# Kernel tuning notes

Measured on AMD Instinct MI355X. Metric: run time of the kernel, lower is better.

## Reference

```python
import jax, jax.numpy as jnp
import numpy as np

H = 768   # encoder hidden size
NH = 4    # boundary attention heads
HD = H // NH
E = 9     # ent_type_size
R = 12    # rel_type_size
D = 64    # inner_dim
B = 4
S = 1024


def setup_inputs() -> dict:
    key = jax.random.key(0)
    ks = jax.random.split(key, 8)
    n = lambda k, shp: jax.random.normal(k, shp, jnp.float32) * 0.02
    return dict(
        hidden_states=jax.random.normal(ks[0], (B, S, H), jnp.float32),
        attention_mask=jnp.ones((B, S), jnp.float32),
        in_proj_w=n(ks[1], (3 * H, H)), in_proj_b=jnp.zeros((3 * H,), jnp.float32),
        out_proj_w=n(ks[2], (H, H)), out_proj_b=jnp.zeros((H,), jnp.float32),
        gate_w=n(ks[3], (H, H)), gate_b=jnp.zeros((H,), jnp.float32),
        ln_g=jnp.ones((H,), jnp.float32), ln_b=jnp.zeros((H,), jnp.float32),
        ent_w=n(ks[4], (E * 2 * D, H)), ent_b=jnp.zeros((E * 2 * D,), jnp.float32),
        prior_w=n(ks[5], (H, E)), prior_b=jnp.zeros((H,), jnp.float32),
        rel_w=n(ks[6], (R * 2 * D, 2 * H)), rel_b=jnp.zeros((R * 2 * D,), jnp.float32),
    )


def _sinusoidal_pos_emb(seq_len, dim, dtype):
    pos = jnp.arange(seq_len, dtype=dtype)[:, None]                 # [S,1]
    inv = jnp.power(jnp.asarray(10000.0, dtype), -2.0 * jnp.arange(dim // 2, dtype=dtype) / dim)
    ang = pos * inv                                                  # [S,D/2]
    emb = jnp.stack([jnp.sin(ang), jnp.cos(ang)], axis=-1).reshape(seq_len, dim)  # [sin0,cos0,sin1,cos1,...]
    return emb


def _gp_matrix(hs, W, b, mask):
    # hs: [B,S,Hin], W: [T*2D, Hin], mask: [B,S]
    bsz, seq_len, _ = hs.shape
    out = hs @ W.T + b                                               # [B,S,T*2D]
    T = out.shape[-1] // (2 * D)
    out = out.reshape(bsz, seq_len, T, 2 * D)
    qw, kw = out[..., :D], out[..., D:]                              # [B,S,T,D]
    # RoPE
    pe = _sinusoidal_pos_emb(seq_len, D, hs.dtype)                   # [S,D]
    cos = jnp.repeat(pe[:, 1::2], 2, axis=-1)[None, :, None, :]      # [1,S,1,D]
    sin = jnp.repeat(pe[:, ::2], 2, axis=-1)[None, :, None, :]

    def rot(x):
        x2 = jnp.stack([-x[..., 1::2], x[..., ::2]], axis=-1).reshape(x.shape)
        return x * cos + x2 * sin

    qw, kw = rot(qw), rot(kw)
    logits = jnp.einsum('bmtd,bntd->btmn', qw, kw)                   # [B,T,S,S]
    pad = mask[:, None, None, :]                                     # masks key dim
    logits = logits * pad - (1.0 - pad) * 1e12
    tril = jnp.tril(jnp.ones((seq_len, seq_len), logits.dtype), -1)
    logits = logits - tril * 1e12                                    # strictly lower triangle masked
    return logits / jnp.sqrt(jnp.asarray(D, logits.dtype))


def _boundary_attention(hs, mask, in_proj_w, in_proj_b, out_proj_w, out_proj_b,
                        gate_w, gate_b, ln_g, ln_b):
    bsz, seq_len, _ = hs.shape
    qkv = hs @ in_proj_w.T + in_proj_b                               # [B,S,3H]
    q, k, v = jnp.split(qkv, 3, axis=-1)
    q = q.reshape(bsz, seq_len, NH, HD)
    k = k.reshape(bsz, seq_len, NH, HD)
    v = v.reshape(bsz, seq_len, NH, HD)
    scores = jnp.einsum('bqhd,bkhd->bhqk', q, k) / jnp.sqrt(jnp.asarray(HD, hs.dtype))
    key_pad = (mask == 0)[:, None, None, :]                          # [B,1,1,S]
    scores = jnp.where(key_pad, jnp.asarray(-1e9, hs.dtype), scores)
    attn = jax.nn.softmax(scores, axis=-1)
    ctx = jnp.einsum('bhqk,bkhd->bqhd', attn, v).reshape(bsz, seq_len, H)
    attn_out = ctx @ out_proj_w.T + out_proj_b
    gate = jax.nn.sigmoid(attn_out @ gate_w.T + gate_b)
    x = hs + gate * attn_out
    mu = jnp.mean(x, axis=-1, keepdims=True)
    var = jnp.var(x, axis=-1, keepdims=True)
    return (x - mu) / jnp.sqrt(var + 1e-5) * ln_g + ln_b


def reference(hidden_states, attention_mask, in_proj_w, in_proj_b, out_proj_w, out_proj_b,
              gate_w, gate_b, ln_g, ln_b, ent_w, ent_b, prior_w, prior_b, rel_w, rel_b):
    enhanced = _boundary_attention(hidden_states, attention_mask, in_proj_w, in_proj_b,
                                   out_proj_w, out_proj_b, gate_w, gate_b, ln_g, ln_b)
    ent_logits = _gp_matrix(enhanced, ent_w, ent_b, attention_mask)  # [B,E,S,S]
    ent_prior = jnp.max(ent_logits, axis=-1)                          # [B,E,S]
    ent_prior = jnp.swapaxes(ent_prior, 1, 2)                         # [B,S,E]
    prior_feat = jax.nn.relu(ent_prior @ prior_w.T + prior_b)         # [B,S,H]
    rel_hidden = jnp.concatenate([enhanced, prior_feat], axis=-1)     # [B,S,2H]
    rel_logits = _gp_matrix(rel_hidden, rel_w, rel_b, attention_mask) # [B,R,S,S]
    return (ent_logits, rel_logits, enhanced)
```

## Files before the change

### kernel.cpp

```cpp
#include <hip/hip_runtime.h>
#include <math.h>

#define H_   768
#define NH_  4
#define HD_  192
#define E_   9
#define R_   12
#define D_   64
#define B_   4
#define S_   1024
#define H3_  (3 * H_)
#define MBS_ (B_ * S_)

typedef unsigned short u16;
typedef __attribute__((ext_vector_type(4))) int   i32x4;
typedef __attribute__((ext_vector_type(4))) float f32x4;

static const long OUT_REL_OFF = (long)B_ * E_ * S_ * S_;
static const long OUT_ENH_OFF = OUT_REL_OFF + (long)B_ * R_ * S_ * S_;

__device__ __forceinline__ u16 f2bf(float f) {
    unsigned u = __builtin_bit_cast(unsigned, f);
    return (u16)((u + 0x7fffu + ((u >> 16) & 1u)) >> 16);
}
__device__ __forceinline__ float bf2f(u16 h) {
    return __builtin_bit_cast(float, (unsigned)h << 16);
}
__device__ __forceinline__ void gload16(const u16* g, u16* l) {
    __builtin_amdgcn_global_load_lds(
        (__attribute__((address_space(1))) void*)g,
        (__attribute__((address_space(3))) void*)l, 16, 0, 0);
}
__device__ __forceinline__ void mfma_bf16(f32x4& acc, i32x4 a, i32x4 b) {
    asm volatile("v_mfma_f32_16x16x32_bf16 %0, %1, %2, %0"
                 : "+v"(acc) : "v"(a), "v"(b));
}

template<int BM, int BN, int EPI, int OBF, int PIPE>
__global__ __launch_bounds__(256) void gemm_mfma(
    const u16* __restrict__ A, const u16* __restrict__ Bw,
    const float* __restrict__ bias, void* __restrict__ Cv,
    int K, int lda, int ldb, int ldc, int nh,
    long sAb, long sAh, long sBb, long sBh, long sCb, long sCh,
    const float* __restrict__ mask, float scale, float* __restrict__ aux)
{
    constexpr int MI = BM / 32, NJ = BN / 32;
    constexpr int BUFE = (BM + BN) * 64;
    constexpr int LPS  = BM / 32 + BN / 32;
    const int z = blockIdx.z;
    const int zb = z / nh, zh = z - zb * nh;
    A  += zb * sAb + zh * sAh;
    Bw += zb * sBb + zh * sBh;

    const int gx = gridDim.x, gy = gridDim.y;
    int id = blockIdx.y * gx + blockIdx.x;
    const int nwg = gx * gy;
    if ((nwg & 7) == 0) id = (id & 7) * (nwg >> 3) + (id >> 3);
    const int bx = id % gx, by = id / gx;
    const int m0 = by * BM, n0 = bx * BN;

    __shared__ u16 lds[(PIPE ? 2 : 1) * BUFE];

    const int t = threadIdx.x;
    const int lane = t & 63, wid = t >> 6;
    const int wr = wid >> 1, wc = wid & 1;
    const int l16 = lane & 15, l4 = lane >> 4;

    auto stage = [&](int kt, u16* la) {
        u16* lb = la + BM * 64;
        const int k0 = kt << 6;
        #pragma unroll
        for (int i = 0; i < BM / 32; ++i) {
            const int e = i * 256 + t;
            const int row = e >> 3;
            const int c = ((e & 7) ^ (row & 7)) << 3;
            gload16(A + (long)(m0 + row) * lda + k0 + c, la + e * 8);
        }
        #pragma unroll
        for (int i = 0; i < BN / 32; ++i) {
            const int e = i * 256 + t;
            const int row = e >> 3;
            const int c = ((e & 7) ^ (row & 7)) << 3;
            gload16(Bw + (long)(n0 + row) * ldb + k0 + c, lb + e * 8);
        }
    };

    f32x4 acc[MI][NJ];
    #pragma unroll
    for (int mi = 0; mi < MI; ++mi)
        #pragma unroll
        for (int nj = 0; nj < NJ; ++nj)
            #pragma unroll
            for (int q = 0; q < 4; ++q) acc[mi][nj][q] = 0.0f;

    const int nt = K >> 6;

    if (PIPE == 0) {
        stage(0, lds);
        __syncthreads();
        const u16* la = lds;
        const u16* lb = lds + BM * 64;
        i32x4 af[MI][2], bfr[NJ][2];
        #pragma unroll
        for (int mi = 0; mi < MI; ++mi)
            #pragma unroll
            for (int kk = 0; kk < 2; ++kk) {
                const int row = wr * (BM / 2) + mi * 16 + l16;
                af[mi][kk] = *(const i32x4*)&la[row * 64 + ((((kk << 2) + l4) ^ (row & 7)) << 3)];
            }
        #pragma unroll
        for (int nj = 0; nj < NJ; ++nj)
            #pragma unroll
            for (int kk = 0; kk < 2; ++kk) {
                const int row = wc * (BN / 2) + nj * 16 + l16;
                bfr[nj][kk] = *(const i32x4*)&lb[row * 64 + ((((kk << 2) + l4) ^ (row & 7)) << 3)];
            }
        #pragma unroll
        for (int kk = 0; kk < 2; ++kk)
            #pragma unroll
            for (int mi = 0; mi < MI; ++mi)
                #pragma unroll
                for (int nj = 0; nj < NJ; ++nj)
                    mfma_bf16(acc[mi][nj], af[mi][kk], bfr[nj][kk]);
    } else {
        stage(0, lds);
        if (nt > 1) stage(1, lds + BUFE);
        for (int tt = 0; tt < nt; ++tt) {
            if (tt + 1 < nt) {
                if constexpr (LPS == 8) asm volatile("s_waitcnt vmcnt(8)" ::: "memory");
                else if constexpr (LPS == 7) asm volatile("s_waitcnt vmcnt(7)" ::: "memory");
                else if constexpr (LPS == 6) asm volatile("s_waitcnt vmcnt(6)" ::: "memory");
                else asm volatile("s_waitcnt vmcnt(5)" ::: "memory");
            } else {
                asm volatile("s_waitcnt vmcnt(0)" ::: "memory");
            }
            __builtin_amdgcn_s_barrier();
            u16* la = lds + (tt & 1) * BUFE;
            const u16* lb = la + BM * 64;
            i32x4 af[MI][2], bfr[NJ][2];
            #pragma unroll
            for (int mi = 0; mi < MI; ++mi)
                #pragma unroll
                for (int kk = 0; kk < 2; ++kk) {
                    const int row = wr * (BM / 2) + mi * 16 + l16;
                    af[mi][kk] = *(const i32x4*)&la[row * 64 + ((((kk << 2) + l4) ^ (row & 7)) << 3)];
                }
            #pragma unroll
            for (int nj = 0; nj < NJ; ++nj)
                #pragma unroll
                for (int kk = 0; kk < 2; ++kk) {
                    const int row = wc * (BN / 2) + nj * 16 + l16;
                    bfr[nj][kk] = *(const i32x4*)&lb[row * 64 + ((((kk << 2) + l4) ^ (row & 7)) << 3)];
                }
            asm volatile("s_waitcnt lgkmcnt(0)" ::: "memory");
            __builtin_amdgcn_sched_barrier(0);
            __builtin_amdgcn_s_barrier();
            if (tt + 2 < nt) stage(tt + 2, la);
            #pragma unroll
            for (int kk = 0; kk < 2; ++kk)
                #pragma unroll
                for (int mi = 0; mi < MI; ++mi)
                    #pragma unroll
                    for (int nj = 0; nj < NJ; ++nj)
                        mfma_bf16(acc[mi][nj], af[mi][kk], bfr[nj][kk]);
        }
        __syncthreads();
    }
    __builtin_amdgcn_sched_barrier(0);
    asm volatile("s_nop 7");
    asm volatile("s_nop 7");
    __builtin_amdgcn_sched_barrier(0);

    if (EPI == 1 || EPI == 3 || EPI == 5) mask += (long)zb * S_;
    const long cbase = zb * sCb + zh * sCh;

    float* sminv = (float*)lds;
    if (EPI == 6) {
        if (t < BM) {
            const float* pp = aux + ((long)z * S_ + m0 + t) * 16;
            float s = 0.0f;
            #pragma unroll
            for (int i = 0; i < 16; ++i) s += pp[i];
            sminv[t] = 1.0f / s;
        }
        __syncthreads();
    }

    float red[MI][4];
    if (EPI == 3 || EPI == 5) {
        #pragma unroll
        for (int mi = 0; mi < MI; ++mi)
            #pragma unroll
            for (int r = 0; r < 4; ++r) red[mi][r] = (EPI == 3) ? -INFINITY : 0.0f;
    }

    #pragma unroll
    for (int mi = 0; mi < MI; ++mi) {
        #pragma unroll
        for (int nj = 0; nj < NJ; ++nj) {
            const int gn = n0 + wc * (BN / 2) + nj * 16 + l16;
            const float bv = ((EPI == 0 || EPI == 4 || EPI == 7) && bias) ? bias[gn] : 0.0f;
            float invf = 0.0f;
            if (EPI == 4) invf = exp2f(-(float)((gn & 63) >> 1) * 0.41524101186092503f);
            #pragma unroll
            for (int r = 0; r < 4; ++r) {
                const int gm = m0 + wr * (BM / 2) + mi * 16 + l4 * 4 + r;
                float v = acc[mi][nj][r];
                const long cidx = cbase + (long)gm * ldc + gn;
                if (EPI == 0) {
                    v += bv;
                    if (OBF) ((u16*)Cv)[cidx] = f2bf(v);
                    else     ((float*)Cv)[cidx] = v;
                } else if (EPI == 7) {
                    v += bv;
                    const u16 bfv = f2bf(v);
                    ((u16*)Cv)[cidx] = bfv;
                    if (gn >= 2 * H_) {
                        const int hh = (gn - 2 * H_) / HD_;
                        const int dd = (gn - 2 * H_) - hh * HD_;
                        const int bb = gm >> 10, ss = gm & (S_ - 1);
                        ((u16*)aux)[((long)(bb * NH_ + hh) * HD_ + dd) * S_ + ss] = bfv;
                    }
                } else if (EPI == 1 || EPI == 3) {
                    const float pad = mask[gn];
                    v = v * pad - (1.0f - pad) * 1e12f;
                    if (gm > gn) v -= 1e12f;
                    v *= 0.125f;
                    ((float*)Cv)[cidx] = v;
                    if (EPI == 3) red[mi][r] = fmaxf(red[mi][r], v);
                } else if (EPI == 5) {
                    float tv = 0.0f;
                    if (mask[gn] != 0.0f) tv = __expf(v * scale);
                    ((u16*)Cv)[cidx] = f2bf(tv);
                    red[mi][r] += tv;
                } else if (EPI == 6) {
                    v *= sminv[gm - m0];
                    ((u16*)Cv)[cidx] = f2bf(v);
                } else {
                    v += bv;
                    const int sp = gm & (S_ - 1);
                    float sn, cs;
                    __sincosf((float)sp * invf, &sn, &cs);
                    const float pv = __shfl_xor(v, 1, 64);
                    v = (gn & 1) ? fmaf(v, cs, pv * sn) : fmaf(v, cs, -pv * sn);
                    ((u16*)Cv)[cidx] = f2bf(v);
                }
            }
        }
    }

    if (EPI == 3 || EPI == 5) {
        #pragma unroll
        for (int mi = 0; mi < MI; ++mi) {
            #pragma unroll
            for (int r = 0; r < 4; ++r) {
                float m = red[mi][r];
                if (EPI == 3) {
                    m = fmaxf(m, __shfl_xor(m, 1, 64));
                    m = fmaxf(m, __shfl_xor(m, 2, 64));
                    m = fmaxf(m, __shfl_xor(m, 4, 64));
                    m = fmaxf(m, __shfl_xor(m, 8, 64));
                } else {
                    m += __shfl_xor(m, 1, 64);
                    m += __shfl_xor(m, 2, 64);
                    m += __shfl_xor(m, 4, 64);
                    m += __shfl_xor(m, 8, 64);
                }
                if (l16 == 0) {
                    const int gm = m0 + wr * (BM / 2) + mi * 16 + l4 * 4 + r;
                    aux[((long)z * S_ + gm) * 16 + bx * 2 + wc] = m;
                }
            }
        }
    }
}

__global__ __launch_bounds__(256) void cast_all(
    const float* __restrict__ hs, const float* __restrict__ ipw,
    const float* __restrict__ opw, const float* __restrict__ gw,
    const float* __restrict__ entw, const float* __restrict__ relw,
    u16* hs_o, u16* ipw_o, u16* opw_o, u16* gw_o, u16* entw_o, u16* relw_o)
{
    const int blk = blockIdx.x;
    const float* in; u16* out; long base;
    if      (blk < 3072) { in = hs;   out = hs_o;   base = (long)blk * 1024; }
    else if (blk < 4800) { in = ipw;  out = ipw_o;  base = (long)(blk - 3072) * 1024; }
    else if (blk < 5376) { in = opw;  out = opw_o;  base = (long)(blk - 4800) * 1024; }
    else if (blk < 5952) { in = gw;   out = gw_o;   base = (long)(blk - 5376) * 1024; }
    else if (blk < 6816) { in = entw; out = entw_o; base = (long)(blk - 5952) * 1024; }
    else                 { in = relw; out = relw_o; base = (long)(blk - 6816) * 1024; }
    const long idx = base + (long)threadIdx.x * 4;
    const float4 v = *(const float4*)&in[idx];
    ushort4 o; o.x = f2bf(v.x); o.y = f2bf(v.y); o.z = f2bf(v.z); o.w = f2bf(v.w);
    *(ushort4*)&out[idx] = o;
}

__global__ __launch_bounds__(256) void gate_ln_bf(
    const float* __restrict__ hs, const u16* __restrict__ aogl,
    const float* __restrict__ g, const float* __restrict__ bta,
    float* __restrict__ enh, u16* __restrict__ relh)
{
    const long row = blockIdx.x;
    const float* hrow = hs + row * H_;
    const u16* arow = aogl + row * (2 * H_);
    const int tid = threadIdx.x;
    float x[3];
    float sum = 0.0f, sq = 0.0f;
    #pragma unroll
    for (int i = 0; i < 3; ++i) {
        const int j = tid + i * 256;
        const float a = bf2f(arow[j]);
        const float gt = 1.0f / (1.0f + __expf(-bf2f(arow[H_ + j])));
        const float xv = hrow[j] + gt * a;
        x[i] = xv; sum += xv; sq += xv * xv;
    }
    __shared__ float sm[8];
    #pragma unroll
    for (int o = 32; o > 0; o >>= 1) {
        sum += __shfl_xor(sum, o, 64);
        sq  += __shfl_xor(sq, o, 64);
    }
    const int lane = tid & 63, wid = tid >> 6;
    if (lane == 0) { sm[wid] = sum; sm[4 + wid] = sq; }
    __syncthreads();
    sum = sm[0] + sm[1] + sm[2] + sm[3];
    sq  = sm[4] + sm[5] + sm[6] + sm[7];
    const float mu = sum * (1.0f / (float)H_);
    float var = sq * (1.0f / (float)H_) - mu * mu;
    var = fmaxf(var, 0.0f);
    const float inv = 1.0f / sqrtf(var + 1e-5f);
    #pragma unroll
    for (int i = 0; i < 3; ++i) {
        const int j = tid + i * 256;
        const float o = (x[i] - mu) * inv * g[j] + bta[j];
        enh[row * H_ + j] = o;
        relh[row * (2 * H_) + j] = f2bf(o);
    }
}

__global__ __launch_bounds__(256) void prior_fused(
    const float* __restrict__ pmax, const float* __restrict__ pw,
    const float* __restrict__ pb, u16* __restrict__ relh)
{
    const int row = blockIdx.x;
    const int b = row >> 10, m = row & (S_ - 1);
    __shared__ float pr[E_];
    const int tid = threadIdx.x;
    if (tid < E_) {
        const float* pp = pmax + ((long)(b * E_ + tid) * S_ + m) * 16;
        float mx = -INFINITY;
        #pragma unroll
        for (int i = 0; i < 16; ++i) mx = fmaxf(mx, pp[i]);
        pr[tid] = mx;
    }
    __syncthreads();
    float p[E_];
    #pragma unroll
    for (int e = 0; e < E_; ++e) p[e] = pr[e];
    u16* orow = relh + (long)row * (2 * H_) + H_;
    #pragma unroll
    for (int i = 0; i < 3; ++i) {
        const int j = tid + i * 256;
        float a = pb[j];
        #pragma unroll
        for (int e = 0; e < E_; ++e) a = fmaf(p[e], pw[j * E_ + e], a);
        orow[j] = f2bf(fmaxf(a, 0.0f));
    }
}

extern "C" void kernel_launch(void* const* d_in, const int* in_sizes, int n_in,
                              void* d_out, int out_size, void* d_ws, size_t ws_size,
                              hipStream_t stream)
{
    const float* hs   = (const float*)d_in[0];
    const float* mask = (const float*)d_in[1];
    const float* ipw  = (const float*)d_in[2];
    const float* ipb  = (const float*)d_in[3];
    const float* opb  = (const float*)d_in[5];
    const float* gb   = (const float*)d_in[7];
    const float* lng  = (const float*)d_in[8];
    const float* lnb  = (const float*)d_in[9];
    const float* entw = (const float*)d_in[10];
    const float* entb = (const float*)d_in[11];
    const float* prw  = (const float*)d_in[12];
    const float* prb  = (const float*)d_in[13];
    const float* relw = (const float*)d_in[14];
    const float* relb = (const float*)d_in[15];
    const float* opw  = (const float*)d_in[4];
    const float* gw   = (const float*)d_in[6];
    float* out = (float*)d_out;
    char* base = (char*)d_ws;

    u16* ipw_bf  = (u16*)(base + 0);
    u16* opw_bf  = (u16*)(base + 3538944);
    u16* gw_bf   = (u16*)(base + 4718592);
    u16* entw_bf = (u16*)(base + 5898240);
    u16* relw_bf = (u16*)(base + 7667712);
    u16* hs_bf   = (u16*)(base + 12386304);
    u16* qkv_bf  = (u16*)(base + 18677760);
    u16* vt_bf   = (u16*)(base + 37552128);
    u16* sc_bf   = (u16*)(base + 43843584);
    u16* ctx_bf  = (u16*)(base + 77398016);
    u16* aogl_bf = (u16*)(base + 83689472);
    float* bias2 = (float*)(base + 96272384);
    float* psum  = (float*)(base + 96280576);
    float* pmax  = (float*)(base + 97329152);
    u16* relh_bf = (u16*)(base + 18677760);
    u16* projr   = (u16*)(base + 37552128);
    float* enh   = out + OUT_ENH_OFF;

    const float qscale = 0.07216878364870323f;

    hipMemcpyAsync(bias2, opb, H_ * sizeof(float), hipMemcpyDeviceToDevice, stream);
    hipMemcpyAsync(bias2 + H_, gb, H_ * sizeof(float), hipMemcpyDeviceToDevice, stream);

    cast_all<<<9120, 256, 0, stream>>>(hs, ipw, opw, gw, entw, relw,
                                       hs_bf, ipw_bf, opw_bf, gw_bf, entw_bf, relw_bf);

    gemm_mfma<128,96,7,1,1><<<dim3(24, 32, 1), 256, 0, stream>>>(
        hs_bf, ipw_bf, ipb, qkv_bf, H_, H_, H_, H3_, 1,
        0,0,0,0,0,0, nullptr, 0.0f, (float*)vt_bf);

    gemm_mfma<128,128,5,1,1><<<dim3(8, 8, B_ * NH_), 256, 0, stream>>>(
        qkv_bf, qkv_bf + H_, nullptr, sc_bf, HD_, H3_, H3_, S_, NH_,
        (long)S_ * H3_, HD_, (long)S_ * H3_, HD_,
        (long)NH_ * S_ * S_, (long)S_ * S_, mask, qscale, psum);

    gemm_mfma<64,96,6,1,1><<<dim3(2, 16, B_ * NH_), 256, 0, stream>>>(
        sc_bf, vt_bf, nullptr, ctx_bf, S_, S_, S_, H_, NH_,
        (long)NH_ * S_ * S_, (long)S_ * S_, (long)NH_ * HD_ * S_, (long)HD_ * S_,
        (long)S_ * H_, HD_, nullptr, 0.0f, psum);

    gemm_mfma<128,96,0,1,1><<<dim3(16, 32, 1), 256, 0, stream>>>(
        ctx_bf, opw_bf, bias2, aogl_bf, H_, H_, H_, 2 * H_, 1,
        0,0,0,0,0,0, nullptr, 0.0f, nullptr);

    gate_ln_bf<<<MBS_, 256, 0, stream>>>(hs, aogl_bf, lng, lnb, enh, relh_bf);

    gemm_mfma<64,96,4,1,1><<<dim3(12, 64, 1), 256, 0, stream>>>(
        relh_bf, entw_bf, entb, projr, H_, 2 * H_, H_, E_ * 2 * D_, 1,
        0,0,0,0,0,0, nullptr, 0.0f, nullptr);

    gemm_mfma<128,128,3,0,0><<<dim3(8, 8, B_ * E_), 256, 0, stream>>>(
        projr, projr + D_, nullptr, out, D_, E_ * 2 * D_, E_ * 2 * D_, S_, E_,
        (long)S_ * E_ * 2 * D_, 2 * D_, (long)S_ * E_ * 2 * D_, 2 * D_,
        (long)E_ * S_ * S_, (long)S_ * S_, mask, 0.0f, pmax);

    prior_fused<<<MBS_, 256, 0, stream>>>(pmax, prw, prb, relh_bf);

    gemm_mfma<128,96,4,1,1><<<dim3(16, 32, 1), 256, 0, stream>>>(
        relh_bf, relw_bf, relb, projr, 2 * H_, 2 * H_, 2 * H_, R_ * 2 * D_, 1,
        0,0,0,0,0,0, nullptr, 0.0f, nullptr);

    gemm_mfma<128,128,1,0,0><<<dim3(8, 8, B_ * R_), 256, 0, stream>>>(
        projr, projr + D_, nullptr, out + OUT_REL_OFF, D_, R_ * 2 * D_, R_ * 2 * D_, S_, R_,
        (long)S_ * R_ * 2 * D_, 2 * D_, (long)S_ * R_ * 2 * D_, 2 * D_,
        (long)R_ * S_ * S_, (long)S_ * S_, mask, 0.0f, nullptr);

    (void)in_sizes; (void)n_in; (void)out_size; (void)ws_size;
}
```

Baseline: 252.6 us.

## Fuse boundary attention QK^T, softmax and PV into one flash-style kernel

Replaces the two-GEMM attention path, which wrote a bf16 score matrix of B*NH*S*S to global memory and then read it back for the PV GEMM, with a single fused kernel. Each block holds 64 query rows in registers, streams K and V tiles through swizzled LDS, exponentiates the scores, stages P in LDS, and accumulates context and row sums before normalising. The aim is to remove the large score-matrix write and read plus one launch. In exchange the grid is only 256 blocks, each looping serially over 16 KV tiles with barriers and little load/compute overlap, so occupancy and latency hiding may be weaker. Like the original path, the softmax does no max subtraction.

New measurement: 257.6 us. No clear change (+2.0%).

```diff
diff --git a/kernel.cpp b/kernel.cpp
--- a/kernel.cpp
+++ b/kernel.cpp
@@ -171,27 +171,15 @@
     asm volatile("s_nop 7");
     __builtin_amdgcn_sched_barrier(0);
 
-    if (EPI == 1 || EPI == 3 || EPI == 5) mask += (long)zb * S_;
+    if (EPI == 1 || EPI == 3) mask += (long)zb * S_;
     const long cbase = zb * sCb + zh * sCh;
 
-    float* sminv = (float*)lds;
-    if (EPI == 6) {
-        if (t < BM) {
-            const float* pp = aux + ((long)z * S_ + m0 + t) * 16;
-            float s = 0.0f;
-            #pragma unroll
-            for (int i = 0; i < 16; ++i) s += pp[i];
-            sminv[t] = 1.0f / s;
-        }
-        __syncthreads();
-    }
-
     float red[MI][4];
-    if (EPI == 3 || EPI == 5) {
+    if (EPI == 3) {
         #pragma unroll
         for (int mi = 0; mi < MI; ++mi)
             #pragma unroll
-            for (int r = 0; r < 4; ++r) red[mi][r] = (EPI == 3) ? -INFINITY : 0.0f;
+            for (int r = 0; r < 4; ++r) red[mi][r] = -INFINITY;
     }
 
     #pragma unroll
@@ -228,14 +216,6 @@
                     v *= 0.125f;
                     ((float*)Cv)[cidx] = v;
                     if (EPI == 3) red[mi][r] = fmaxf(red[mi][r], v);
-                } else if (EPI == 5) {
-                    float tv = 0.0f;
-                    if (mask[gn] != 0.0f) tv = __expf(v * scale);
-                    ((u16*)Cv)[cidx] = f2bf(tv);
-                    red[mi][r] += tv;
-                } else if (EPI == 6) {
-                    v *= sminv[gm - m0];
-                    ((u16*)Cv)[cidx] = f2bf(v);
                 } else {
                     v += bv;
                     const int sp = gm & (S_ - 1);
@@ -249,27 +229,191 @@
         }
     }
 
-    if (EPI == 3 || EPI == 5) {
+    if (EPI == 3) {
         #pragma unroll
         for (int mi = 0; mi < MI; ++mi) {
             #pragma unroll
             for (int r = 0; r < 4; ++r) {
                 float m = red[mi][r];
-                if (EPI == 3) {
-                    m = fmaxf(m, __shfl_xor(m, 1, 64));
-                    m = fmaxf(m, __shfl_xor(m, 2, 64));
-                    m = fmaxf(m, __shfl_xor(m, 4, 64));
-                    m = fmaxf(m, __shfl_xor(m, 8, 64));
-                } else {
-                    m += __shfl_xor(m, 1, 64);
-                    m += __shfl_xor(m, 2, 64);
-                    m += __shfl_xor(m, 4, 64);
-                    m += __shfl_xor(m, 8, 64);
-                }
+                m = fmaxf(m, __shfl_xor(m, 1, 64));
+                m = fmaxf(m, __shfl_xor(m, 2, 64));
+                m = fmaxf(m, __shfl_xor(m, 4, 64));
+                m = fmaxf(m, __shfl_xor(m, 8, 64));
                 if (l16 == 0) {
                     const int gm = m0 + wr * (BM / 2) + mi * 16 + l4 * 4 + r;
                     aux[((long)z * S_ + gm) * 16 + bx * 2 + wc] = m;
                 }
+            }
+        }
+    }
+}
+
+__global__ __launch_bounds__(256) void attn_fused(
+    const u16* __restrict__ qkv, const u16* __restrict__ vt,
+    const float* __restrict__ mask, u16* __restrict__ ctx, float qscale)
+{
+    const int z = blockIdx.y;
+    const int b = z >> 2, h = z & 3;
+    const int s0 = blockIdx.x * 64;
+    const int t = threadIdx.x;
+    const int lane = t & 63, wid = t >> 6;
+    const int wr = wid >> 1, wc = wid & 1;
+    const int l16 = lane & 15, l4 = lane >> 4;
+
+    __shared__ u16 k_lds[64 * 192];
+    __shared__ u16 v_lds[192 * 64];
+    __shared__ u16 p_lds[64 * 64];
+    __shared__ float rs_lds[2][64];
+
+    i32x4 qf[2][6];
+    {
+        const u16* qb = qkv + (long)(b * S_ + s0 + wr * 32 + l16) * H3_ + h * HD_;
+        #pragma unroll
+        for (int mi = 0; mi < 2; ++mi)
+            #pragma unroll
+            for (int kk = 0; kk < 6; ++kk)
+                qf[mi][kk] = *(const i32x4*)(qb + (long)mi * 16 * H3_ + kk * 32 + l4 * 8);
+    }
+    asm volatile("s_waitcnt vmcnt(0)" ::: "memory");
+
+    f32x4 acc_c[2][6];
+    #pragma unroll
+    for (int mi = 0; mi < 2; ++mi)
+        #pragma unroll
+        for (int nj = 0; nj < 6; ++nj)
+            #pragma unroll
+            for (int q = 0; q < 4; ++q) acc_c[mi][nj][q] = 0.0f;
+    float rs_acc[2][4] = {};
+
+    const float* mrow = mask + (long)b * S_;
+
+    for (int kt = 0; kt < 16; ++kt) {
+        const int kv0 = kt * 64;
+        #pragma unroll
+        for (int i = 0; i < 6; ++i) {
+            const int e = i * 256 + t;
+            const int row = e / 24;
+            const int g = e - row * 24;
+            const int gs = (g & ~7) | ((g & 7) ^ (row & 7));
+            gload16(qkv + (long)(b * S_ + kv0 + row) * H3_ + H_ + h * HD_ + gs * 8,
+                    k_lds + e * 8);
+        }
+        #pragma unroll
+        for (int i = 0; i < 6; ++i) {
+            const int e = i * 256 + t;
+            const int row = e >> 3, g = e & 7;
+            const int gs = g ^ (row & 7);
+            gload16(vt + ((long)z * HD_ + row) * S_ + kv0 + gs * 8,
+                    v_lds + e * 8);
+        }
+        asm volatile("s_waitcnt vmcnt(6)" ::: "memory");
+        __builtin_amdgcn_s_barrier();
+
+        f32x4 acc_s[2][2];
+        #pragma unroll
+        for (int mi = 0; mi < 2; ++mi)
+            #pragma unroll
+            for (int nj = 0; nj < 2; ++nj)
+                #pragma unroll
+                for (int q = 0; q < 4; ++q) acc_s[mi][nj][q] = 0.0f;
+        #pragma unroll
+        for (int kk = 0; kk < 6; ++kk) {
+            #pragma unroll
+            for (int nj = 0; nj < 2; ++nj) {
+                const int row = wc * 32 + nj * 16 + l16;
+                const int g = kk * 4 + l4;
+                const int gs = (g & ~7) | ((g & 7) ^ (row & 7));
+                const i32x4 kf = *(const i32x4*)&k_lds[row * 192 + gs * 8];
+                #pragma unroll
+                for (int mi = 0; mi < 2; ++mi)
+                    mfma_bf16(acc_s[mi][nj], qf[mi][kk], kf);
+            }
+        }
+        __builtin_amdgcn_sched_barrier(0);
+        asm volatile("s_nop 7");
+        asm volatile("s_nop 7");
+        __builtin_amdgcn_sched_barrier(0);
+
+        float rsp[2][4] = {};
+        #pragma unroll
+        for (int mi = 0; mi < 2; ++mi) {
+            #pragma unroll
+            for (int nj = 0; nj < 2; ++nj) {
+                const int coll = wc * 32 + nj * 16 + l16;
+                const float mk = mrow[kv0 + coll];
+                #pragma unroll
+                for (int r = 0; r < 4; ++r) {
+                    const int rowl = wr * 32 + mi * 16 + l4 * 4 + r;
+                    float tv = 0.0f;
+                    if (mk != 0.0f) tv = __expf(acc_s[mi][nj][r] * qscale);
+                    const int gs = (coll >> 3) ^ (rowl & 7);
+                    p_lds[rowl * 64 + gs * 8 + (coll & 7)] = f2bf(tv);
+                    rsp[mi][r] += tv;
+                }
+            }
+        }
+        #pragma unroll
+        for (int mi = 0; mi < 2; ++mi)
+            #pragma unroll
+            for (int r = 0; r < 4; ++r) {
+                float v = rsp[mi][r];
+                v += __shfl_xor(v, 1, 64);
+                v += __shfl_xor(v, 2, 64);
+                v += __shfl_xor(v, 4, 64);
+                v += __shfl_xor(v, 8, 64);
+                rs_acc[mi][r] += v;
+            }
+
+        asm volatile("s_waitcnt vmcnt(0)" ::: "memory");
+        __builtin_amdgcn_s_barrier();
+
+        #pragma unroll
+        for (int kk = 0; kk < 2; ++kk) {
+            i32x4 pf[2];
+            #pragma unroll
+            for (int mi = 0; mi < 2; ++mi) {
+                const int row = wr * 32 + mi * 16 + l16;
+                const int gs = (kk * 4 + l4) ^ (row & 7);
+                pf[mi] = *(const i32x4*)&p_lds[row * 64 + gs * 8];
+            }
+            #pragma unroll
+            for (int nj = 0; nj < 6; ++nj) {
+                const int row = wc * 96 + nj * 16 + l16;
+                const int gs = (kk * 4 + l4) ^ (row & 7);
+                const i32x4 vf = *(const i32x4*)&v_lds[row * 64 + gs * 8];
+                #pragma unroll
+                for (int mi = 0; mi < 2; ++mi)
+                    mfma_bf16(acc_c[mi][nj], pf[mi], vf);
+            }
+        }
+        __builtin_amdgcn_s_barrier();
+    }
+
+    __builtin_amdgcn_sched_barrier(0);
+    asm volatile("s_nop 7");
+    asm volatile("s_nop 7");
+    __builtin_amdgcn_sched_barrier(0);
+
+    if (l16 == 0) {
+        #pragma unroll
+        for (int mi = 0; mi < 2; ++mi)
+            #pragma unroll
+            for (int r = 0; r < 4; ++r)
+                rs_lds[wc][wr * 32 + mi * 16 + l4 * 4 + r] = rs_acc[mi][r];
+    }
+    __syncthreads();
+
+    #pragma unroll
+    for (int mi = 0; mi < 2; ++mi) {
+        #pragma unroll
+        for (int r = 0; r < 4; ++r) {
+            const int rowl = wr * 32 + mi * 16 + l4 * 4 + r;
+            const float inv = 1.0f / (rs_lds[0][rowl] + rs_lds[1][rowl]);
+            #pragma unroll
+            for (int nj = 0; nj < 6; ++nj) {
+                const int d = wc * 96 + nj * 16 + l16;
+                ctx[(long)(b * S_ + s0 + rowl) * H_ + h * HD_ + d] =
+                    f2bf(acc_c[mi][nj][r] * inv);
             }
         }
     }
@@ -376,7 +520,9 @@
     const float* mask = (const float*)d_in[1];
     const float* ipw  = (const float*)d_in[2];
     const float* ipb  = (const float*)d_in[3];
+    const float* opw  = (const float*)d_in[4];
     const float* opb  = (const float*)d_in[5];
+    const float* gw   = (const float*)d_in[6];
     const float* gb   = (const float*)d_in[7];
     const float* lng  = (const float*)d_in[8];
     const float* lnb  = (const float*)d_in[9];
@@ -386,8 +532,6 @@
     const float* prb  = (const float*)d_in[13];
     const float* relw = (const float*)d_in[14];
     const float* relb = (const float*)d_in[15];
-    const float* opw  = (const float*)d_in[4];
-    const float* gw   = (const float*)d_in[6];
     float* out = (float*)d_out;
     char* base = (char*)d_ws;
 
@@ -399,14 +543,12 @@
     u16* hs_bf   = (u16*)(base + 12386304);
     u16* qkv_bf  = (u16*)(base + 18677760);
     u16* vt_bf   = (u16*)(base + 37552128);
-    u16* sc_bf   = (u16*)(base + 43843584);
     u16* ctx_bf  = (u16*)(base + 77398016);
     u16* aogl_bf = (u16*)(base + 83689472);
     float* bias2 = (float*)(base + 96272384);
-    float* psum  = (float*)(base + 96280576);
     float* pmax  = (float*)(base + 97329152);
-    u16* relh_bf = (u16*)(base + 18677760);
-    u16* projr   = (u16*)(base + 37552128);
+    u16* relh_bf = (u16*)(base + 43843584);
+    u16* projr   = (u16*)(base + 56426496);
     float* enh   = out + OUT_ENH_OFF;
 
     const float qscale = 0.07216878364870323f;
@@ -421,15 +563,8 @@
         hs_bf, ipw_bf, ipb, qkv_bf, H_, H_, H_, H3_, 1,
         0,0,0,0,0,0, nullptr, 0.0f, (float*)vt_bf);
 
-    gemm_mfma<128,128,5,1,1><<<dim3(8, 8, B_ * NH_), 256, 0, stream>>>(
-        qkv_bf, qkv_bf + H_, nullptr, sc_bf, HD_, H3_, H3_, S_, NH_,
-        (long)S_ * H3_, HD_, (long)S_ * H3_, HD_,
-        (long)NH_ * S_ * S_, (long)S_ * S_, mask, qscale, psum);
-
-    gemm_mfma<64,96,6,1,1><<<dim3(2, 16, B_ * NH_), 256, 0, stream>>>(
-        sc_bf, vt_bf, nullptr, ctx_bf, S_, S_, S_, H_, NH_,
-        (long)NH_ * S_ * S_, (long)S_ * S_, (long)NH_ * HD_ * S_, (long)HD_ * S_,
-        (long)S_ * H_, HD_, nullptr, 0.0f, psum);
+    attn_fused<<<dim3(16, 16), 256, 0, stream>>>(
+        qkv_bf, vt_bf, mask, ctx_bf, qscale);
 
     gemm_mfma<128,96,0,1,1><<<dim3(16, 32, 1), 256, 0, stream>>>(
         ctx_bf, opw_bf, bias2, aogl_bf, H_, H_, H_, 2 * H_, 1,
```
